# Kernel optimization log

Hardware: AMD Instinct MI355X
Metric: run time of the kernel (lower is better)

The kernel has to match this reference:

```python
import jax, jax.numpy as jnp
import numpy as np

B, S, HID, H = 2, 2048, 1024, 16
D = HID // H
MAX_SEQ = 2048
NEG = -1e9


def setup_inputs() -> dict:
    key = jax.random.key(0)
    ks = jax.random.split(key, 12)
    s = 0.02
    inp = {
        'query': jax.random.normal(ks[0], (B, S, HID), jnp.float32),
        'key_in': jax.random.normal(ks[1], (B, S, HID), jnp.float32),
        'value': jax.random.normal(ks[2], (B, S, HID), jnp.float32),
        # causal mask so every row has at least one valid key
        'attn_mask': jnp.tril(jnp.ones((S, S), bool))[None].repeat(B, axis=0),
        'wq': jax.random.normal(ks[3], (HID, HID), jnp.float32) * s,
        'bq': jnp.zeros((HID,), jnp.float32),
        'wk': jax.random.normal(ks[4], (HID, HID), jnp.float32) * s,
        'bk': jnp.zeros((HID,), jnp.float32),
        'wv': jax.random.normal(ks[5], (HID, HID), jnp.float32) * s,
        'bv': jnp.zeros((HID,), jnp.float32),
        'wo': jax.random.normal(ks[6], (HID, HID), jnp.float32) * s,
        'bo': jnp.zeros((HID,), jnp.float32),
        'rel_emb': jax.random.normal(ks[7], (2 * MAX_SEQ - 1, H), jnp.float32) * s,
    }
    return inp


def _rope_tables(seq_len, dim):
    inv_freq = 1.0 / (10000.0 ** (jnp.arange(0, dim, 2, dtype=jnp.float32) / dim))
    t = jnp.arange(seq_len, dtype=jnp.float32)
    freqs = t[:, None] * inv_freq[None, :]          # [S, D/2]
    emb = jnp.concatenate([freqs, freqs], axis=-1)  # [S, D]
    return jnp.cos(emb), jnp.sin(emb)


def _apply_rope(x, cos, sin):
    # x: [B,H,S,D]; faithful to source: gather even/odd strides, concat(-odd, even)
    x_even = x[..., 0::2]
    x_odd = x[..., 1::2]
    x_rot = jnp.concatenate([-x_odd, x_even], axis=-1)
    return x * cos + x_rot * sin


def reference(query, key_in, value, attn_mask, wq, bq, wk, bk, wv, bv, wo, bo, rel_emb):
    Bq, Sq, _ = query.shape
    Q = query @ wq.T + bq
    K = key_in @ wk.T + bk
    V = value @ wv.T + bv
    Q = Q.reshape(Bq, Sq, H, D).transpose(0, 2, 1, 3)  # [B,H,S,D]
    K = K.reshape(Bq, Sq, H, D).transpose(0, 2, 1, 3)
    V = V.reshape(Bq, Sq, H, D).transpose(0, 2, 1, 3)

    cos, sin = _rope_tables(Sq, D)
    Q = _apply_rope(Q, cos, sin)
    K = _apply_rope(K, cos, sin)

    # relative position bias: gather [S,S,H] -> [1,H,S,S]
    pos = jnp.arange(Sq)[:, None] - jnp.arange(Sq)[None, :]
    rel_idx = pos + MAX_SEQ - 1
    rel_bias = rel_emb[rel_idx].transpose(2, 0, 1)[None]  # [1,H,S,S]

    float_mask = jnp.where(attn_mask, 0.0, NEG)[:, None]  # [B,1,S,S]
    bias = float_mask + rel_bias                            # [B,H,S,S]

    scale = D ** -0.5
    scores = jnp.einsum('bhqd,bhkd->bhqk', Q, K) * scale + bias
    attn = jax.nn.softmax(scores, axis=-1)
    out = jnp.einsum('bhqk,bhkd->bhqd', attn, V)            # [B,H,S,D]
    out = out.transpose(0, 2, 1, 3).reshape(Bq, Sq, HID)
    out = jnp.clip(out, -30.0, 30.0)
    return out @ wo.T + bo
```

## Files before the change

### kernel.cpp

```cpp
#include <hip/hip_runtime.h>


typedef __attribute__((ext_vector_type(8))) short short8;
typedef __attribute__((ext_vector_type(4))) short short4v;
typedef __attribute__((ext_vector_type(4))) float f32x4;

__device__ __forceinline__ float bf2f(unsigned short u) {
  return __uint_as_float(((unsigned int)u) << 16);
}
__device__ __forceinline__ unsigned short f2bf(float f) {
  unsigned int u = __float_as_uint(f);
  u += 0x7fffu + ((u >> 16) & 1u);
  return (unsigned short)(u >> 16);
}

#define GLL16(gp, lp) __builtin_amdgcn_global_load_lds( \
    (const __attribute__((address_space(1))) void*)(gp), \
    (__attribute__((address_space(3))) void*)(lp), 16, 0, 0)

#define MFMA16(a, b, c) __builtin_amdgcn_mfma_f32_16x16x32_bf16((a), (b), (c), 0, 0, 0)

__global__ __launch_bounds__(256) void prep_kernel(
    const float* __restrict__ q, const float* __restrict__ k,
    const float* __restrict__ v,
    const float* __restrict__ wq, const float* __restrict__ wk,
    const float* __restrict__ wv, const float* __restrict__ wo,
    unsigned short* __restrict__ xq, unsigned short* __restrict__ xk,
    unsigned short* __restrict__ xv,
    unsigned short* __restrict__ wqb, unsigned short* __restrict__ wkb,
    unsigned short* __restrict__ wvb, unsigned short* __restrict__ wob,
    float* __restrict__ tab, float* __restrict__ relt,
    const float* __restrict__ rel)
{
  int tid = blockIdx.x * 256 + threadIdx.x;
  if (tid < 2097152) {
    const float* src; unsigned short* dst; size_t off;
    if (tid < 1572864) {
      int seg = tid / 524288, rc = tid - seg * 524288;
      src = seg == 0 ? q : (seg == 1 ? k : v);
      dst = seg == 0 ? xq : (seg == 1 ? xk : xv);
      off = (size_t)rc * 8;
    } else {
      int c2 = tid - 1572864;
      int seg = c2 / 131072, rc = c2 - seg * 131072;
      src = seg == 0 ? wq : (seg == 1 ? wk : (seg == 2 ? wv : wo));
      dst = seg == 0 ? wqb : (seg == 1 ? wkb : (seg == 2 ? wvb : wob));
      off = (size_t)rc * 8;
    }
    float4 f0 = ((const float4*)(src + off))[0];
    float4 f1 = ((const float4*)(src + off))[1];
    short8 o;
    o[0]=f2bf(f0.x); o[1]=f2bf(f0.y); o[2]=f2bf(f0.z); o[3]=f2bf(f0.w);
    o[4]=f2bf(f1.x); o[5]=f2bf(f1.y); o[6]=f2bf(f1.z); o[7]=f2bf(f1.w);
    *(short8*)(dst + off) = o;
  } else if (tid < 2162688) {
    int u = tid - 2097152;
    int s = u >> 5, j = u & 31;
    float f = expf((float)j * -0.28782313662425575f);
    float sn, cs;
    sincosf((float)s * f, &sn, &cs);
    tab[s * 64 + j] = cs;
    tab[s * 64 + 32 + j] = sn;
  } else {
    int u = tid - 2162688;
    int hh = u >> 12, d = u & 4095;
    if (d < 4095) relt[hh * 4095 + d] = rel[d * 16 + hh];
  }
}

template<bool SWAP>
__device__ __forceinline__ void core128x64(
    const unsigned short* gA, const unsigned short* gB,
    unsigned short* As, unsigned short* Bs,
    f32x4 (&acc)[4][2], int t, int wm, int wn, int lid, int quad)
{
  for (int k0 = 0; k0 < 1024; k0 += 32) {
    __syncthreads();
    GLL16(gA + k0,         As + t * 8);
    GLL16(gA + 65536 + k0, As + 2048 + t * 8);
    GLL16(gB + k0,         Bs + t * 8);
    __syncthreads();
    short8 af[4], bf[2];
#pragma unroll
    for (int i = 0; i < 4; i++)
      af[i] = *(const short8*)(As + (wm + i * 16 + lid) * 32 + quad * 8);
#pragma unroll
    for (int j = 0; j < 2; j++)
      bf[j] = *(const short8*)(Bs + (wn + j * 16 + lid) * 32 + quad * 8);
#pragma unroll
    for (int i = 0; i < 4; i++)
#pragma unroll
      for (int j = 0; j < 2; j++)
        acc[i][j] = SWAP ? MFMA16(bf[j], af[i], acc[i][j])
                         : MFMA16(af[i], bf[j], acc[i][j]);
  }
}

__global__ __launch_bounds__(256) void gemm_qkv(
    const unsigned short* __restrict__ Xq, const unsigned short* __restrict__ Xk,
    const unsigned short* __restrict__ Xv,
    const unsigned short* __restrict__ Wq, const unsigned short* __restrict__ Wk,
    const unsigned short* __restrict__ Wv,
    const float* __restrict__ bq, const float* __restrict__ bk,
    const float* __restrict__ bv,
    unsigned short* __restrict__ Qr, unsigned short* __restrict__ Kr,
    unsigned short* __restrict__ Vtr)
{
  __shared__ unsigned short As[128 * 32];
  __shared__ unsigned short Bs[64 * 32];
  const int z = blockIdx.z;
  const unsigned short* X = z == 0 ? Xq : (z == 1 ? Xk : Xv);
  const unsigned short* W = z == 0 ? Wq : (z == 1 ? Wk : Wv);
  const float* Bi = z == 0 ? bq : (z == 1 ? bk : bv);
  unsigned short* O = z == 0 ? Qr : (z == 1 ? Kr : Vtr);

  const int t    = threadIdx.x;
  const int lane = t & 63;
  const int lid  = lane & 15;
  const int quad = lane >> 4;
  const int w    = t >> 6;
  const int wm   = (w >> 1) * 64;
  const int wn   = (w & 1) * 32;
  const int m0   = blockIdx.y * 128;
  const int n0   = blockIdx.x * 64;

  const unsigned short* gA = X + (size_t)(m0 + (t >> 2)) * 1024 + (t & 3) * 8;
  const unsigned short* gB = W + (size_t)(n0 + (t >> 2)) * 1024 + (t & 3) * 8;

  f32x4 acc[4][2];
#pragma unroll
  for (int i = 0; i < 4; i++)
#pragma unroll
    for (int j = 0; j < 2; j++) acc[i][j] = (f32x4){0.f, 0.f, 0.f, 0.f};

  if (z == 2) core128x64<false>(gA, gB, As, Bs, acc, t, wm, wn, lid, quad);
  else        core128x64<true >(gA, gB, As, Bs, acc, t, wm, wn, lid, quad);

  if (z < 2) {
#pragma unroll
    for (int jn = 0; jn < 2; jn++) {
      int nn = n0 + wn + jn * 16 + quad * 4;
      int hh = nn >> 6, d0 = nn & 63;
      float4 b4 = *(const float4*)(Bi + nn);
#pragma unroll
      for (int im = 0; im < 4; im++) {
        int m = m0 + wm + im * 16 + lid;
        int bb = m >> 11, s = m & 2047;
        short4v pk;
        pk[0] = (short)f2bf(acc[im][jn][0] + b4.x);
        pk[1] = (short)f2bf(acc[im][jn][1] + b4.y);
        pk[2] = (short)f2bf(acc[im][jn][2] + b4.z);
        pk[3] = (short)f2bf(acc[im][jn][3] + b4.w);
        *(short4v*)(O + ((size_t)((bb * 16 + hh) * 2048 + s)) * 64 + d0) = pk;
      }
    }
  } else {
#pragma unroll
    for (int j = 0; j < 2; j++) {
      int n = n0 + wn + j * 16 + lid;
      int hh = n >> 6, d = n & 63;
      float bvv = Bi[n];
#pragma unroll
      for (int i = 0; i < 4; i++) {
        int mr = m0 + wm + i * 16 + quad * 4;
        int bb = mr >> 11, s0 = mr & 2047;
        short4v pk;
        pk[0] = (short)f2bf(acc[i][j][0] + bvv);
        pk[1] = (short)f2bf(acc[i][j][1] + bvv);
        pk[2] = (short)f2bf(acc[i][j][2] + bvv);
        pk[3] = (short)f2bf(acc[i][j][3] + bvv);
        *(short4v*)(O + ((size_t)((bb * 16 + hh) * 64 + d)) * 2048 + s0) = pk;
      }
    }
  }
}

__global__ __launch_bounds__(256) void gemm_out(
    const unsigned short* __restrict__ X, const unsigned short* __restrict__ W,
    const float* __restrict__ Bi, float* __restrict__ O)
{
  __shared__ unsigned short As[64 * 32];
  __shared__ unsigned short Bs[64 * 32];
  const int t    = threadIdx.x;
  const int lane = t & 63;
  const int lid  = lane & 15;
  const int quad = lane >> 4;
  const int w    = t >> 6;
  const int wm   = (w >> 1) * 32;
  const int wn   = (w & 1) * 32;
  const int m0   = blockIdx.y * 64;
  const int n0   = blockIdx.x * 64;

  const unsigned short* gA = X + (size_t)(m0 + (t >> 2)) * 1024 + (t & 3) * 8;
  const unsigned short* gB = W + (size_t)(n0 + (t >> 2)) * 1024 + (t & 3) * 8;

  f32x4 acc[2][2];
#pragma unroll
  for (int i = 0; i < 2; i++)
#pragma unroll
    for (int j = 0; j < 2; j++) acc[i][j] = (f32x4){0.f, 0.f, 0.f, 0.f};

  for (int k0 = 0; k0 < 1024; k0 += 32) {
    __syncthreads();
    GLL16(gA + k0, As + t * 8);
    GLL16(gB + k0, Bs + t * 8);
    __syncthreads();
    short8 af[2], bf[2];
#pragma unroll
    for (int i = 0; i < 2; i++)
      af[i] = *(const short8*)(As + (wm + i * 16 + lid) * 32 + quad * 8);
#pragma unroll
    for (int j = 0; j < 2; j++)
      bf[j] = *(const short8*)(Bs + (wn + j * 16 + lid) * 32 + quad * 8);
#pragma unroll
    for (int i = 0; i < 2; i++)
#pragma unroll
      for (int j = 0; j < 2; j++)
        acc[i][j] = MFMA16(bf[j], af[i], acc[i][j]);
  }
#pragma unroll
  for (int jn = 0; jn < 2; jn++) {
    int nn = n0 + wn + jn * 16 + quad * 4;
    float4 b4 = *(const float4*)(Bi + nn);
#pragma unroll
    for (int im = 0; im < 2; im++) {
      int m = m0 + wm + im * 16 + lid;
      float4 ov;
      ov.x = acc[im][jn][0] + b4.x;
      ov.y = acc[im][jn][1] + b4.y;
      ov.z = acc[im][jn][2] + b4.z;
      ov.w = acc[im][jn][3] + b4.w;
      *(float4*)(O + (size_t)m * 1024 + nn) = ov;
    }
  }
}

__global__ __launch_bounds__(256) void rope_kernel(unsigned short* __restrict__ Q,
                                                   unsigned short* __restrict__ Kp,
                                                   const float* __restrict__ tab)
{
  int row = blockIdx.x * 256 + threadIdx.x;
  unsigned short* P = ((blockIdx.y == 0) ? Q : Kp) + (size_t)row * 64;
  const float* tr = tab + (size_t)(row & 2047) * 64;

  short8 xv[8];
#pragma unroll
  for (int c = 0; c < 8; c++) xv[c] = *(const short8*)(P + c * 8);
#define XE(i) bf2f((unsigned short)xv[(i) >> 3][(i) & 7])
  short8 ov[8];
#pragma unroll
  for (int j = 0; j < 32; j++) {
    float cs = tr[j], sn = tr[32 + j];
    float yl = XE(j) * cs      - XE(2 * j + 1) * sn;
    float yh = XE(j + 32) * cs + XE(2 * j)     * sn;
    ov[j >> 3][j & 7]       = (short)f2bf(yl);
    ov[(j >> 3) + 4][j & 7] = (short)f2bf(yh);
  }
#undef XE
#pragma unroll
  for (int c = 0; c < 8; c++) *(short8*)(P + c * 8) = ov[c];
}

__global__ __launch_bounds__(64, 2) void attn_kernel(
    const unsigned short* __restrict__ Q, const unsigned short* __restrict__ Kg,
    const unsigned short* __restrict__ Vt, const float* __restrict__ relt,
    unsigned short* __restrict__ AO)
{
  __shared__ unsigned short Ps[32 * 72];

  const int lane = threadIdx.x;
  const int lid  = lane & 15;
  const int quad = lane >> 4;
  const int jid  = blockIdx.x;
  const int bh   = jid >> 6;
  const int p    = jid & 63;
  const int h    = bh & 15;
  const int qA   = 2032 - 16 * p;
  const int qB   = 16 * p;
  const int kendA = qA + 16, kendB = qB + 16;

  const unsigned short* Qb = Q  + (size_t)bh * (2048 * 64);
  const unsigned short* Kb = Kg + (size_t)bh * (2048 * 64);
  const unsigned short* Vb = Vt + (size_t)bh * (64 * 2048);
  const float* relh = relt + h * 4095 + 2047;
  unsigned short* AOb = AO + (size_t)(bh >> 4) * (2048 * 1024) + h * 64;

  short8 aqA[2], aqB[2];
  {
    const unsigned short* qp = Qb + (size_t)(qA + lid) * 64;
    aqA[0] = *(const short8*)(qp + quad * 8);
    aqA[1] = *(const short8*)(qp + 32 + quad * 8);
    qp = Qb + (size_t)(qB + lid) * 64;
    aqB[0] = *(const short8*)(qp + quad * 8);
    aqB[1] = *(const short8*)(qp + 32 + quad * 8);
  }

  f32x4 accA[4], accB[4];
  float lA[4] = {0.f, 0.f, 0.f, 0.f}, lB[4] = {0.f, 0.f, 0.f, 0.f};
#pragma unroll
  for (int dj = 0; dj < 4; dj++) {
    accA[dj] = (f32x4){0.f, 0.f, 0.f, 0.f};
    accB[dj] = (f32x4){0.f, 0.f, 0.f, 0.f};
  }

  const unsigned short* kr = Kb + (size_t)lid * 64 + quad * 8;
  const unsigned short* vr = Vb + (size_t)lid * 2048 + quad * 8;

  short8 ck[4][2], nk[4][2], cv[4][2];

  auto loadK = [&](short8 (&fk)[4][2], int k0) {
#pragma unroll
    for (int x = 0; x < 4; x++) {
      const unsigned short* kp = kr + (size_t)(k0 + x * 16) * 64;
      fk[x][0] = *(const short8*)kp;
      fk[x][1] = *(const short8*)(kp + 32);
    }
  };
  auto loadV = [&](short8 (&fv)[4][2], int k0) {
#pragma unroll
    for (int x = 0; x < 4; x++) {
      const unsigned short* vp = vr + (size_t)(x * 16) * 2048 + k0;
      fv[x][0] = *(const short8*)vp;
      fv[x][1] = *(const short8*)(vp + 32);
    }
  };
  auto proc = [&](const short8 (&aq)[2], f32x4 (&acc)[4], float (&l)[4],
                  int qr0, int k0, const short8 (&fk)[4][2],
                  const short8 (&fv)[4][2], int pbase) {
    f32x4 s4[4];
#pragma unroll
    for (int jt = 0; jt < 4; jt++) {
      s4[jt] = (f32x4){0.f, 0.f, 0.f, 0.f};
      s4[jt] = MFMA16(aq[0], fk[jt][0], s4[jt]);
      s4[jt] = MFMA16(aq[1], fk[jt][1], s4[jt]);
    }
#pragma unroll
    for (int jt = 0; jt < 4; jt++) {
      int kb = k0 + jt * 16 + lid;
      const float* rp = relh + (qr0 - kb);
#pragma unroll
      for (int r = 0; r < 4; r++) {
        float sc = fmaf(s4[jt][r], 0.125f, rp[r]);
        float pv = (kb > qr0 + r) ? 0.f : __expf(sc);
        l[r] += pv;
        Ps[(pbase + quad * 4 + r) * 72 + jt * 16 + lid] = f2bf(pv);
      }
    }
    short8 ap0 = *(const short8*)(Ps + (pbase + lid) * 72 + quad * 8);
    short8 ap1 = *(const short8*)(Ps + (pbase + lid) * 72 + 32 + quad * 8);
#pragma unroll
    for (int dj = 0; dj < 4; dj++) {
      acc[dj] = MFMA16(ap0, fv[dj][0], acc[dj]);
      acc[dj] = MFMA16(ap1, fv[dj][1], acc[dj]);
    }
  };

  const int qrA = qA + quad * 4, qrB = qB + quad * 4;
  int k0 = 0;
  loadK(ck, 0);
  while (true) {
    int k1 = k0 + 64;
    if (k1 < kendA) loadK(nk, k1);
    loadV(cv, k0);
    proc(aqA, accA, lA, qrA, k0, ck, cv, 0);
    if (k0 < kendB) proc(aqB, accB, lB, qrB, k0, ck, cv, 16);
    if (k1 >= kendA) break;
    k0 = k1; k1 = k0 + 64;
    if (k1 < kendA) loadK(ck, k1);
    loadV(cv, k0);
    proc(aqA, accA, lA, qrA, k0, nk, cv, 0);
    if (k0 < kendB) proc(aqB, accB, lB, qrB, k0, nk, cv, 16);
    if (k1 >= kendA) break;
    k0 = k1;
  }

#pragma unroll
  for (int d2 = 1; d2 < 16; d2 <<= 1)
#pragma unroll
    for (int r = 0; r < 4; r++) {
      lA[r] += __shfl_xor(lA[r], d2);
      lB[r] += __shfl_xor(lB[r], d2);
    }
#pragma unroll
  for (int r = 0; r < 4; r++) {
    float rA = 1.f / lA[r], rB = 1.f / lB[r];
#pragma unroll
    for (int dj = 0; dj < 4; dj++) {
      float vA = fminf(fmaxf(accA[dj][r] * rA, -30.f), 30.f);
      float vB = fminf(fmaxf(accB[dj][r] * rB, -30.f), 30.f);
      AOb[(size_t)(qrA + r) * 1024 + dj * 16 + lid] = f2bf(vA);
      AOb[(size_t)(qrB + r) * 1024 + dj * 16 + lid] = f2bf(vB);
    }
  }
}

extern "C" void kernel_launch(void* const* d_in, const int* in_sizes, int n_in,
                              void* d_out, int out_size, void* d_ws, size_t ws_size,
                              hipStream_t stream) {
  const float* query  = (const float*)d_in[0];
  const float* key_in = (const float*)d_in[1];
  const float* value  = (const float*)d_in[2];
  const float* wq = (const float*)d_in[4];
  const float* bq = (const float*)d_in[5];
  const float* wk = (const float*)d_in[6];
  const float* bk = (const float*)d_in[7];
  const float* wv = (const float*)d_in[8];
  const float* bv = (const float*)d_in[9];
  const float* wo = (const float*)d_in[10];
  const float* bo = (const float*)d_in[11];
  const float* rel = (const float*)d_in[12];

  char* ws = (char*)d_ws;
  unsigned short* Xq = (unsigned short*)(ws);
  unsigned short* Xk = (unsigned short*)(ws + 8388608);
  unsigned short* Xv = (unsigned short*)(ws + 16777216);
  unsigned short* Wq = (unsigned short*)(ws + 25165824);
  unsigned short* Wk = (unsigned short*)(ws + 27262976);
  unsigned short* Wv = (unsigned short*)(ws + 29360128);
  unsigned short* Wo = (unsigned short*)(ws + 31457280);
  unsigned short* Qr  = (unsigned short*)(ws + 33554432);
  unsigned short* Kr  = (unsigned short*)(ws + 41943040);
  unsigned short* Vtr = (unsigned short*)(ws + 50331648);
  unsigned short* AOp = Xq;
  float* out  = (float*)d_out;
  float* tab  = out;
  float* relt = out + 131072;

  dim3 blk(256);
  prep_kernel<<<dim3(8704), blk, 0, stream>>>(
      query, key_in, value, wq, wk, wv, wo,
      Xq, Xk, Xv, Wq, Wk, Wv, Wo, tab, relt, rel);
  gemm_qkv<<<dim3(16, 32, 3), blk, 0, stream>>>(
      Xq, Xk, Xv, Wq, Wk, Wv, bq, bk, bv, Qr, Kr, Vtr);
  rope_kernel<<<dim3(256, 2), blk, 0, stream>>>(Qr, Kr, tab);
  attn_kernel<<<dim3(2048), dim3(64), 0, stream>>>(Qr, Kr, Vtr, relt, AOp);
  gemm_out<<<dim3(16, 64), blk, 0, stream>>>(AOp, Wo, bo, out);
}
```

Measured before the change: 352.0 us.

## Split causal attention into key-range partials with a separate reduction kernel

Replaces the paired-row attention kernel (one wave handling a short and a long query tile) with a split-K scheme. Query tiles past row 1024 are split into two key halves, giving 192 work items per head, and each item writes unnormalized fp32 partial outputs and row sums. A new reduce kernel adds the partials, normalizes, clips and writes the bf16 attention output. The aim is more parallelism and higher occupancy (launch bounds raised to 4, smaller LDS), paid for with extra global traffic for the partials and one more kernel launch.

After: 480.2 us. +36.4%, slower.

```diff
diff --git a/kernel.cpp b/kernel.cpp
--- a/kernel.cpp
+++ b/kernel.cpp
@@ -261,53 +261,48 @@
   for (int c = 0; c < 8; c++) *(short8*)(P + c * 8) = ov[c];
 }
 
-__global__ __launch_bounds__(64, 2) void attn_kernel(
+__global__ __launch_bounds__(64, 4) void attn_partial(
     const unsigned short* __restrict__ Q, const unsigned short* __restrict__ Kg,
     const unsigned short* __restrict__ Vt, const float* __restrict__ relt,
-    unsigned short* __restrict__ AO)
-{
-  __shared__ unsigned short Ps[32 * 72];
+    float* __restrict__ Opart, float* __restrict__ Lpart)
+{
+  __shared__ unsigned short Ps[16 * 72];
 
   const int lane = threadIdx.x;
   const int lid  = lane & 15;
   const int quad = lane >> 4;
-  const int jid  = blockIdx.x;
-  const int bh   = jid >> 6;
-  const int p    = jid & 63;
+  const int er   = 191 - blockIdx.x;
+  const int bh   = blockIdx.y;
   const int h    = bh & 15;
-  const int qA   = 2032 - 16 * p;
-  const int qB   = 16 * p;
-  const int kendA = qA + 16, kendB = qB + 16;
+  int p, s;
+  if (er < 64) { p = er; s = 0; }
+  else { int u = er - 64; p = 64 + (u >> 1); s = u & 1; }
+  const int slot = bh * 192 + er;
+  const int q0   = 16 * p;
+  const int k_lo = s << 10;
+  const int k_hi = min(q0 + 16, (s + 1) << 10);
 
   const unsigned short* Qb = Q  + (size_t)bh * (2048 * 64);
   const unsigned short* Kb = Kg + (size_t)bh * (2048 * 64);
   const unsigned short* Vb = Vt + (size_t)bh * (64 * 2048);
   const float* relh = relt + h * 4095 + 2047;
-  unsigned short* AOb = AO + (size_t)(bh >> 4) * (2048 * 1024) + h * 64;
-
-  short8 aqA[2], aqB[2];
+
+  short8 aq[2];
   {
-    const unsigned short* qp = Qb + (size_t)(qA + lid) * 64;
-    aqA[0] = *(const short8*)(qp + quad * 8);
-    aqA[1] = *(const short8*)(qp + 32 + quad * 8);
-    qp = Qb + (size_t)(qB + lid) * 64;
-    aqB[0] = *(const short8*)(qp + quad * 8);
-    aqB[1] = *(const short8*)(qp + 32 + quad * 8);
-  }
-
-  f32x4 accA[4], accB[4];
-  float lA[4] = {0.f, 0.f, 0.f, 0.f}, lB[4] = {0.f, 0.f, 0.f, 0.f};
-#pragma unroll
-  for (int dj = 0; dj < 4; dj++) {
-    accA[dj] = (f32x4){0.f, 0.f, 0.f, 0.f};
-    accB[dj] = (f32x4){0.f, 0.f, 0.f, 0.f};
-  }
+    const unsigned short* qp = Qb + (size_t)(q0 + lid) * 64;
+    aq[0] = *(const short8*)(qp + quad * 8);
+    aq[1] = *(const short8*)(qp + 32 + quad * 8);
+  }
+
+  f32x4 acc[4];
+  float l[4] = {0.f, 0.f, 0.f, 0.f};
+#pragma unroll
+  for (int dj = 0; dj < 4; dj++) acc[dj] = (f32x4){0.f, 0.f, 0.f, 0.f};
 
   const unsigned short* kr = Kb + (size_t)lid * 64 + quad * 8;
   const unsigned short* vr = Vb + (size_t)lid * 2048 + quad * 8;
 
   short8 ck[4][2], nk[4][2], cv[4][2];
-
   auto loadK = [&](short8 (&fk)[4][2], int k0) {
 #pragma unroll
     for (int x = 0; x < 4; x++) {
@@ -324,9 +319,8 @@
       fv[x][1] = *(const short8*)(vp + 32);
     }
   };
-  auto proc = [&](const short8 (&aq)[2], f32x4 (&acc)[4], float (&l)[4],
-                  int qr0, int k0, const short8 (&fk)[4][2],
-                  const short8 (&fv)[4][2], int pbase) {
+  const int qr0 = q0 + quad * 4;
+  auto proc = [&](int k0, const short8 (&fk)[4][2], const short8 (&fv)[4][2]) {
     f32x4 s4[4];
 #pragma unroll
     for (int jt = 0; jt < 4; jt++) {
@@ -343,11 +337,11 @@
         float sc = fmaf(s4[jt][r], 0.125f, rp[r]);
         float pv = (kb > qr0 + r) ? 0.f : __expf(sc);
         l[r] += pv;
-        Ps[(pbase + quad * 4 + r) * 72 + jt * 16 + lid] = f2bf(pv);
+        Ps[(quad * 4 + r) * 72 + jt * 16 + lid] = f2bf(pv);
       }
     }
-    short8 ap0 = *(const short8*)(Ps + (pbase + lid) * 72 + quad * 8);
-    short8 ap1 = *(const short8*)(Ps + (pbase + lid) * 72 + 32 + quad * 8);
+    short8 ap0 = *(const short8*)(Ps + lid * 72 + quad * 8);
+    short8 ap1 = *(const short8*)(Ps + lid * 72 + 32 + quad * 8);
 #pragma unroll
     for (int dj = 0; dj < 4; dj++) {
       acc[dj] = MFMA16(ap0, fv[dj][0], acc[dj]);
@@ -355,43 +349,66 @@
     }
   };
 
-  const int qrA = qA + quad * 4, qrB = qB + quad * 4;
-  int k0 = 0;
-  loadK(ck, 0);
+  int k0 = k_lo;
+  loadK(ck, k0);
   while (true) {
     int k1 = k0 + 64;
-    if (k1 < kendA) loadK(nk, k1);
+    if (k1 < k_hi) loadK(nk, k1);
     loadV(cv, k0);
-    proc(aqA, accA, lA, qrA, k0, ck, cv, 0);
-    if (k0 < kendB) proc(aqB, accB, lB, qrB, k0, ck, cv, 16);
-    if (k1 >= kendA) break;
+    proc(k0, ck, cv);
+    if (k1 >= k_hi) break;
     k0 = k1; k1 = k0 + 64;
-    if (k1 < kendA) loadK(ck, k1);
+    if (k1 < k_hi) loadK(ck, k1);
     loadV(cv, k0);
-    proc(aqA, accA, lA, qrA, k0, nk, cv, 0);
-    if (k0 < kendB) proc(aqB, accB, lB, qrB, k0, nk, cv, 16);
-    if (k1 >= kendA) break;
+    proc(k0, nk, cv);
+    if (k1 >= k_hi) break;
     k0 = k1;
   }
 
 #pragma unroll
   for (int d2 = 1; d2 < 16; d2 <<= 1)
 #pragma unroll
-    for (int r = 0; r < 4; r++) {
-      lA[r] += __shfl_xor(lA[r], d2);
-      lB[r] += __shfl_xor(lB[r], d2);
-    }
-#pragma unroll
-  for (int r = 0; r < 4; r++) {
-    float rA = 1.f / lA[r], rB = 1.f / lB[r];
-#pragma unroll
-    for (int dj = 0; dj < 4; dj++) {
-      float vA = fminf(fmaxf(accA[dj][r] * rA, -30.f), 30.f);
-      float vB = fminf(fmaxf(accB[dj][r] * rB, -30.f), 30.f);
-      AOb[(size_t)(qrA + r) * 1024 + dj * 16 + lid] = f2bf(vA);
-      AOb[(size_t)(qrB + r) * 1024 + dj * 16 + lid] = f2bf(vB);
-    }
-  }
+    for (int r = 0; r < 4; r++) l[r] += __shfl_xor(l[r], d2);
+
+  float* Ob = Opart + (size_t)slot * 1024;
+#pragma unroll
+  for (int dj = 0; dj < 4; dj++)
+#pragma unroll
+    for (int r = 0; r < 4; r++)
+      Ob[(quad * 4 + r) * 64 + dj * 16 + lid] = acc[dj][r];
+  if (lid == 0) {
+#pragma unroll
+    for (int r = 0; r < 4; r++) Lpart[slot * 16 + quad * 4 + r] = l[r];
+  }
+}
+
+__global__ __launch_bounds__(256) void attn_reduce(
+    const float* __restrict__ Opart, const float* __restrict__ Lpart,
+    unsigned short* __restrict__ AO)
+{
+  const int p  = blockIdx.x;
+  const int bh = blockIdx.y;
+  const int t  = threadIdx.x;
+  const int er0  = (p < 64) ? p : 64 + ((p - 64) << 1);
+  const int slot = bh * 192 + er0;
+  const int row = t >> 4, d0 = (t & 15) * 4;
+
+  const float* O0 = Opart + (size_t)slot * 1024 + row * 64 + d0;
+  float4 a = *(const float4*)O0;
+  float l = Lpart[slot * 16 + row];
+  if (p >= 64) {
+    float4 a2 = *(const float4*)(O0 + 1024);
+    a.x += a2.x; a.y += a2.y; a.z += a2.z; a.w += a2.w;
+    l += Lpart[(slot + 1) * 16 + row];
+  }
+  float rcp = 1.f / l;
+  short4v pk;
+  pk[0] = (short)f2bf(fminf(fmaxf(a.x * rcp, -30.f), 30.f));
+  pk[1] = (short)f2bf(fminf(fmaxf(a.y * rcp, -30.f), 30.f));
+  pk[2] = (short)f2bf(fminf(fmaxf(a.z * rcp, -30.f), 30.f));
+  pk[3] = (short)f2bf(fminf(fmaxf(a.w * rcp, -30.f), 30.f));
+  int qrow = 16 * p + row;
+  *(short4v*)(AO + ((size_t)(bh >> 4) * 2048 + qrow) * 1024 + (bh & 15) * 64 + d0) = pk;
 }
 
 extern "C" void kernel_launch(void* const* d_in, const int* in_sizes, int n_in,
@@ -421,7 +438,9 @@
   unsigned short* Qr  = (unsigned short*)(ws + 33554432);
   unsigned short* Kr  = (unsigned short*)(ws + 41943040);
   unsigned short* Vtr = (unsigned short*)(ws + 50331648);
-  unsigned short* AOp = Xq;
+  float* Opart = (float*)ws;
+  float* Lpart = (float*)(ws + 25165824);
+  unsigned short* AOp = Qr;
   float* out  = (float*)d_out;
   float* tab  = out;
   float* relt = out + 131072;
@@ -433,6 +452,8 @@
   gemm_qkv<<<dim3(16, 32, 3), blk, 0, stream>>>(
       Xq, Xk, Xv, Wq, Wk, Wv, bq, bk, bv, Qr, Kr, Vtr);
   rope_kernel<<<dim3(256, 2), blk, 0, stream>>>(Qr, Kr, tab);
-  attn_kernel<<<dim3(2048), dim3(64), 0, stream>>>(Qr, Kr, Vtr, relt, AOp);
+  attn_partial<<<dim3(192, 32), dim3(64), 0, stream>>>(Qr, Kr, Vtr, relt,
+                                                       Opart, Lpart);
+  attn_reduce<<<dim3(128, 32), blk, 0, stream>>>(Opart, Lpart, AOp);
   gemm_out<<<dim3(16, 64), blk, 0, stream>>>(AOp, Wo, bo, out);
 }
```

## Compute transposed scores so P stays in registers, dropping the LDS round-trip

Applied to the files above, without the earlier changes.

Swaps the MFMA operand order so each lane holds a query column of S^T, letting the exp'd probabilities be packed directly into the B operand of 16x16x16 MFMAs against V. This removes the shared-memory P staging buffer and its store/load traffic, shrinks the row-sum reduction to two shuffles, and vectorizes the output stores. In exchange it uses twice as many smaller-K MFMA instructions for PV and narrower 8-byte V loads.

After: 406.1 us. 1.15x slower.

```diff
diff --git a/kernel.cpp b/kernel.cpp
--- a/kernel.cpp
+++ b/kernel.cpp
@@ -18,7 +18,8 @@
     (const __attribute__((address_space(1))) void*)(gp), \
     (__attribute__((address_space(3))) void*)(lp), 16, 0, 0)
 
-#define MFMA16(a, b, c) __builtin_amdgcn_mfma_f32_16x16x32_bf16((a), (b), (c), 0, 0, 0)
+#define MFMA16(a, b, c)  __builtin_amdgcn_mfma_f32_16x16x32_bf16((a), (b), (c), 0, 0, 0)
+#define MFMAK16(a, b, c) __builtin_amdgcn_mfma_f32_16x16x16bf16_1k((a), (b), (c), 0, 0, 0)
 
 __global__ __launch_bounds__(256) void prep_kernel(
     const float* __restrict__ q, const float* __restrict__ k,
@@ -266,8 +267,6 @@
     const unsigned short* __restrict__ Vt, const float* __restrict__ relt,
     unsigned short* __restrict__ AO)
 {
-  __shared__ unsigned short Ps[32 * 72];
-
   const int lane = threadIdx.x;
   const int lid  = lane & 15;
   const int quad = lane >> 4;
@@ -296,7 +295,7 @@
   }
 
   f32x4 accA[4], accB[4];
-  float lA[4] = {0.f, 0.f, 0.f, 0.f}, lB[4] = {0.f, 0.f, 0.f, 0.f};
+  float lA = 0.f, lB = 0.f;
 #pragma unroll
   for (int dj = 0; dj < 4; dj++) {
     accA[dj] = (f32x4){0.f, 0.f, 0.f, 0.f};
@@ -304,9 +303,10 @@
   }
 
   const unsigned short* kr = Kb + (size_t)lid * 64 + quad * 8;
-  const unsigned short* vr = Vb + (size_t)lid * 2048 + quad * 8;
-
-  short8 ck[4][2], nk[4][2], cv[4][2];
+  const unsigned short* vr = Vb + (size_t)lid * 2048 + quad * 4;
+
+  short8 ck[4][2], nk[4][2];
+  short4v cv[4][4];
 
   auto loadK = [&](short8 (&fk)[4][2], int k0) {
 #pragma unroll
@@ -316,81 +316,73 @@
       fk[x][1] = *(const short8*)(kp + 32);
     }
   };
-  auto loadV = [&](short8 (&fv)[4][2], int k0) {
-#pragma unroll
-    for (int x = 0; x < 4; x++) {
-      const unsigned short* vp = vr + (size_t)(x * 16) * 2048 + k0;
-      fv[x][0] = *(const short8*)vp;
-      fv[x][1] = *(const short8*)(vp + 32);
-    }
+  auto loadV = [&](int k0) {
+#pragma unroll
+    for (int dj = 0; dj < 4; dj++)
+#pragma unroll
+      for (int jt = 0; jt < 4; jt++)
+        cv[dj][jt] = *(const short4v*)(vr + (size_t)(dj * 16) * 2048 + k0 + jt * 16);
   };
-  auto proc = [&](const short8 (&aq)[2], f32x4 (&acc)[4], float (&l)[4],
-                  int qr0, int k0, const short8 (&fk)[4][2],
-                  const short8 (&fv)[4][2], int pbase) {
+  auto proc = [&](const short8 (&aq)[2], f32x4 (&acc)[4], float& l,
+                  int q0, int k0, const short8 (&fk)[4][2]) {
+    const int qabs = q0 + lid;
     f32x4 s4[4];
 #pragma unroll
     for (int jt = 0; jt < 4; jt++) {
       s4[jt] = (f32x4){0.f, 0.f, 0.f, 0.f};
-      s4[jt] = MFMA16(aq[0], fk[jt][0], s4[jt]);
-      s4[jt] = MFMA16(aq[1], fk[jt][1], s4[jt]);
+      s4[jt] = MFMA16(fk[jt][0], aq[0], s4[jt]);
+      s4[jt] = MFMA16(fk[jt][1], aq[1], s4[jt]);
     }
 #pragma unroll
     for (int jt = 0; jt < 4; jt++) {
-      int kb = k0 + jt * 16 + lid;
-      const float* rp = relh + (qr0 - kb);
+      int kbase = k0 + jt * 16 + quad * 4;
+      const float* rp = relh + (qabs - kbase);
+      short4v pk;
 #pragma unroll
       for (int r = 0; r < 4; r++) {
-        float sc = fmaf(s4[jt][r], 0.125f, rp[r]);
-        float pv = (kb > qr0 + r) ? 0.f : __expf(sc);
-        l[r] += pv;
-        Ps[(pbase + quad * 4 + r) * 72 + jt * 16 + lid] = f2bf(pv);
+        float sc = fmaf(s4[jt][r], 0.125f, rp[-r]);
+        float pv = (kbase + r > qabs) ? 0.f : __expf(sc);
+        l += pv;
+        pk[r] = (short)f2bf(pv);
       }
-    }
-    short8 ap0 = *(const short8*)(Ps + (pbase + lid) * 72 + quad * 8);
-    short8 ap1 = *(const short8*)(Ps + (pbase + lid) * 72 + 32 + quad * 8);
-#pragma unroll
-    for (int dj = 0; dj < 4; dj++) {
-      acc[dj] = MFMA16(ap0, fv[dj][0], acc[dj]);
-      acc[dj] = MFMA16(ap1, fv[dj][1], acc[dj]);
+#pragma unroll
+      for (int dj = 0; dj < 4; dj++)
+        acc[dj] = MFMAK16(cv[dj][jt], pk, acc[dj]);
     }
   };
 
-  const int qrA = qA + quad * 4, qrB = qB + quad * 4;
   int k0 = 0;
   loadK(ck, 0);
   while (true) {
     int k1 = k0 + 64;
     if (k1 < kendA) loadK(nk, k1);
-    loadV(cv, k0);
-    proc(aqA, accA, lA, qrA, k0, ck, cv, 0);
-    if (k0 < kendB) proc(aqB, accB, lB, qrB, k0, ck, cv, 16);
+    loadV(k0);
+    proc(aqA, accA, lA, qA, k0, ck);
+    if (k0 < kendB) proc(aqB, accB, lB, qB, k0, ck);
     if (k1 >= kendA) break;
     k0 = k1; k1 = k0 + 64;
     if (k1 < kendA) loadK(ck, k1);
-    loadV(cv, k0);
-    proc(aqA, accA, lA, qrA, k0, nk, cv, 0);
-    if (k0 < kendB) proc(aqB, accB, lB, qrB, k0, nk, cv, 16);
+    loadV(k0);
+    proc(aqA, accA, lA, qA, k0, nk);
+    if (k0 < kendB) proc(aqB, accB, lB, qB, k0, nk);
     if (k1 >= kendA) break;
     k0 = k1;
   }
 
-#pragma unroll
-  for (int d2 = 1; d2 < 16; d2 <<= 1)
+  lA += __shfl_xor(lA, 16); lA += __shfl_xor(lA, 32);
+  lB += __shfl_xor(lB, 16); lB += __shfl_xor(lB, 32);
+  float rA = 1.f / lA, rB = 1.f / lB;
+#pragma unroll
+  for (int dj = 0; dj < 4; dj++) {
+    short4v oA, oB;
 #pragma unroll
     for (int r = 0; r < 4; r++) {
-      lA[r] += __shfl_xor(lA[r], d2);
-      lB[r] += __shfl_xor(lB[r], d2);
-    }
-#pragma unroll
-  for (int r = 0; r < 4; r++) {
-    float rA = 1.f / lA[r], rB = 1.f / lB[r];
-#pragma unroll
-    for (int dj = 0; dj < 4; dj++) {
-      float vA = fminf(fmaxf(accA[dj][r] * rA, -30.f), 30.f);
-      float vB = fminf(fmaxf(accB[dj][r] * rB, -30.f), 30.f);
-      AOb[(size_t)(qrA + r) * 1024 + dj * 16 + lid] = f2bf(vA);
-      AOb[(size_t)(qrB + r) * 1024 + dj * 16 + lid] = f2bf(vB);
-    }
+      oA[r] = (short)f2bf(fminf(fmaxf(accA[dj][r] * rA, -30.f), 30.f));
+      oB[r] = (short)f2bf(fminf(fmaxf(accB[dj][r] * rB, -30.f), 30.f));
+    }
+    int d0 = dj * 16 + quad * 4;
+    *(short4v*)(AOb + (size_t)(qA + lid) * 1024 + d0) = oA;
+    *(short4v*)(AOb + (size_t)(qB + lid) * 1024 + d0) = oB;
   }
 }
 
```
